# Performance work log

Hardware: AMD Instinct MI355X
Metric: run time of the kernel (lower is better)

## Reference

```python
import jax, jax.numpy as jnp
import numpy as np

DIM_M = 512
NEG_INF = -1e30


def setup_inputs() -> dict:
    key = jax.random.key(0)
    k1, k2, k3, k4, k5, k6, k7 = jax.random.split(key, 7)
    B, Lc, Lq, d = 16, 1024, 512, DIM_M
    C = jax.random.normal(k1, (B, Lc, d), dtype=jnp.float32)
    Q = jax.random.normal(k2, (B, Lq, d), dtype=jnp.float32)
    cmask = jax.random.randint(k3, (B, Lc), 0, 2).astype(jnp.float32)
    qmask = jax.random.randint(k4, (B, Lq), 0, 2).astype(jnp.float32)
    lim = np.sqrt(1.0 / d)
    w = jax.random.uniform(k5, (3 * d,), minval=-lim, maxval=lim, dtype=jnp.float32)
    # out_linear: Linear(4d -> d), torch default init
    bound = np.sqrt(1.0 / (4 * d))
    out_w = jax.random.uniform(k6, (d, 4 * d), minval=-bound, maxval=bound, dtype=jnp.float32)
    out_b = jax.random.uniform(k7, (d,), minval=-bound, maxval=bound, dtype=jnp.float32)
    return {"C": C, "Q": Q, "cmask": cmask, "qmask": qmask, "w": w, "out_w": out_w, "out_b": out_b}


def _mask_logits(t, m):
    return t * m + (1.0 - m) * NEG_INF


def reference(C, Q, cmask, qmask, w, out_w, out_b):
    d = C.shape[-1]
    w1, w2, w3 = w[:d], w[d:2 * d], w[2 * d:]
    # Decomposed trilinear similarity (same math as cat([Ct,Qt,Ct*Qt]) @ w):
    # S[b,i,j] = C[b,i]@w1 + Q[b,j]@w2 + (C[b,i]*w3) @ Q[b,j]
    S = (C @ w1)[:, :, None] + (Q @ w2)[:, None, :] \
        + jnp.einsum('bid,bjd->bij', C * w3, Q)  # [B, Lc, Lq]
    qm = qmask[:, None, :]  # [B, 1, Lq]
    cm = cmask[:, :, None]  # [B, Lc, 1]
    S1 = jax.nn.softmax(_mask_logits(S, qm), axis=2)  # over Lq
    S2 = jax.nn.softmax(_mask_logits(S, cm), axis=1)  # over Lc
    A = jnp.einsum('bij,bjd->bid', S1, Q)  # [B, Lc, d]
    # bmm(bmm(S1, S2^T), C) == S1 @ (S2^T @ C) by associativity (cheaper)
    S2TC = jnp.einsum('bij,bid->bjd', S2, C)  # [B, Lq, d]
    Bm = jnp.einsum('bij,bjd->bid', S1, S2TC)  # [B, Lc, d]
    out = jnp.concatenate([C, A, C * A, C * Bm], axis=2)  # [B, Lc, 4d]
    # dropout inactive (inference); out_linear
    return out @ out_w.T + out_b
```

## Files before the change

### kernel.cpp

```cpp
#include <hip/hip_runtime.h>
#include <hip/hip_bf16.h>


#define NB 16
#define LC 1024
#define LQ 512
#define DM 512
#define D4 2048
#define NEGINF (-1e30f)

typedef __bf16 v8bf __attribute__((ext_vector_type(8)));
typedef __bf16 v4bf __attribute__((ext_vector_type(4)));
typedef float  v4f  __attribute__((ext_vector_type(4)));

#define MFMA16 __builtin_amdgcn_mfma_f32_16x16x32_bf16

#define GLOAD16(gp, lp) __builtin_amdgcn_global_load_lds( \
    (const __attribute__((address_space(1))) void*)(gp), \
    (__attribute__((address_space(3))) void*)(lp), 16, 0, 0)

#define GEMM_PROLOG \
  __shared__ __bf16 Al[128 * 64], Bl[128 * 64]; \
  int bx = blockIdx.x, by = blockIdx.y, bz = blockIdx.z; \
  xcd_remap(bx, by, bz); \
  const int b = bz, i0 = by * 128, n0 = bx * 128; \
  const int t = threadIdx.x, lane = t & 63, wave = t >> 6; \
  const int wm = wave >> 1, wn = wave & 1, quad = lane >> 4, col = lane & 15; \
  const int srow = wave * 32 + (lane >> 3), scol = (lane & 7) * 8; \
  v4f acc[4][4]; \
  _Pragma("unroll") for (int x = 0; x < 4; ++x) \
  _Pragma("unroll") for (int y = 0; y < 4; ++y) \
  _Pragma("unroll") for (int r = 0; r < 4; ++r) acc[x][y][r] = 0.f;

#define GEMM_KLOOP(Arow, Brow, LDGA, LDGB, KEXT) \
  for (int k0 = 0; k0 < (KEXT); k0 += 64) { \
    _Pragma("unroll") for (int u = 0; u < 4; ++u) { \
      GLOAD16(Arow + (size_t)(u * 8) * (LDGA) + k0, &Al[(wave * 32 + u * 8) * 64]); \
      GLOAD16(Brow + (size_t)(u * 8) * (LDGB) + k0, &Bl[(wave * 32 + u * 8) * 64]); \
    } \
    __syncthreads(); \
    _Pragma("unroll") for (int ko = 0; ko < 2; ++ko) { \
      v8bf af_[4], bf_[4]; \
      _Pragma("unroll") for (int x = 0; x < 4; ++x) \
        af_[x] = *(const v8bf*)&Al[(wm * 64 + x * 16 + col) * 64 + ko * 32 + quad * 8]; \
      _Pragma("unroll") for (int y = 0; y < 4; ++y) \
        bf_[y] = *(const v8bf*)&Bl[(wn * 64 + y * 16 + col) * 64 + ko * 32 + quad * 8]; \
      _Pragma("unroll") for (int x = 0; x < 4; ++x) \
      _Pragma("unroll") for (int y = 0; y < 4; ++y) \
        acc[x][y] = MFMA16(af_[x], bf_[y], acc[x][y], 0, 0, 0); \
    } \
    __syncthreads(); \
  }

__device__ __forceinline__ void xcd_remap(int& bx, int& by, int& bz) {
  const int gx = gridDim.x, gy = gridDim.y, gz = gridDim.z;
  int flat = bx + gx * (by + gy * bz);
  int per = (gx * gy * gz) >> 3;
  int nw = (flat & 7) * per + (flat >> 3);
  bx = nw % gx;
  int r = nw / gx;
  by = r % gy;
  bz = r / gy;
}

__global__ void k_rowdots(const float* __restrict__ C, const float* __restrict__ Q,
                          const float* __restrict__ w,
                          float* __restrict__ cw1, float* __restrict__ qw2,
                          __bf16* __restrict__ Cbf, __bf16* __restrict__ Qw3) {
  const int wid = threadIdx.x >> 6, lane = threadIdx.x & 63;
  const int row = blockIdx.x * 4 + wid;
  const bool isC = row < NB * LC;
  const int lr = isC ? row : row - NB * LC;
  const float* src = (isC ? C : Q) + (size_t)lr * DM;
  const float* wv  = isC ? w : (w + DM);
  const float* w3  = w + 2 * DM;
  __bf16* dst = (isC ? Cbf : Qw3) + (size_t)lr * DM;
  float v = 0.f;
#pragma unroll
  for (int s = 0; s < 2; ++s) {
    const int k = lane * 4 + s * 256;
    float4 f = *(const float4*)(src + k);
    float4 g = *(const float4*)(wv + k);
    v += f.x * g.x + f.y * g.y + f.z * g.z + f.w * g.w;
    v4bf h;
    if (isC) {
      h[0] = (__bf16)f.x; h[1] = (__bf16)f.y; h[2] = (__bf16)f.z; h[3] = (__bf16)f.w;
    } else {
      float4 s3 = *(const float4*)(w3 + k);
      h[0] = (__bf16)(f.x * s3.x); h[1] = (__bf16)(f.y * s3.y);
      h[2] = (__bf16)(f.z * s3.z); h[3] = (__bf16)(f.w * s3.w);
    }
    *(v4bf*)(dst + k) = h;
  }
#pragma unroll
  for (int off = 32; off; off >>= 1) v += __shfl_down(v, off, 64);
  if (lane == 0) {
    if (isC) cw1[row] = v;
    else     qw2[lr] = v;
  }
}

__global__ void k_transpose(const float* __restrict__ in, __bf16* __restrict__ outT,
                            int R, int Cd) {
  __shared__ __bf16 tile[64][66];
  const int b = blockIdx.z;
  const int r0 = blockIdx.y * 64, c0 = blockIdx.x * 64;
  const int tr = threadIdx.x >> 6, tc = threadIdx.x & 63;
  const float* inb = in + (size_t)b * R * Cd;
  __bf16* outb = outT + (size_t)b * Cd * R;
  for (int r = tr; r < 64; r += 4)
    tile[r][tc] = (__bf16)inb[(size_t)(r0 + r) * Cd + c0 + tc];
  __syncthreads();
  for (int c = tr; c < 64; c += 4)
    outb[(size_t)(c0 + c) * R + r0 + tc] = tile[tc][c];
}

__global__ void k_cvt2(const float* __restrict__ Cf, const float* __restrict__ OW,
                       __bf16* __restrict__ Cb3, __bf16* __restrict__ OWb) {
  const size_t NC = (size_t)NB * LC * DM;
  size_t i = ((size_t)blockIdx.x * 256 + threadIdx.x) * 4;
  const float* src; __bf16* dst; size_t j;
  if (i < NC) { src = Cf; dst = Cb3; j = i; }
  else        { src = OW; dst = OWb; j = i - NC; }
  float4 f = *(const float4*)(src + j);
  v4bf h; h[0] = (__bf16)f.x; h[1] = (__bf16)f.y; h[2] = (__bf16)f.z; h[3] = (__bf16)f.w;
  *(v4bf*)(dst + j) = h;
}

__global__ __launch_bounds__(256) void k_mfma_S(
    const __bf16* __restrict__ Cbf, const __bf16* __restrict__ Qw3,
    const float* __restrict__ cw1, const float* __restrict__ qw2,
    float* __restrict__ S) {
  GEMM_PROLOG
  const __bf16* Arow = Cbf + (size_t)b * LC * DM + (size_t)(i0 + srow) * DM + scol;
  const __bf16* Brow = Qw3 + (size_t)b * LQ * DM + (size_t)(n0 + srow) * DM + scol;
  GEMM_KLOOP(Arow, Brow, DM, DM, DM)
  float* Sb = S + (size_t)b * LC * LQ;
#pragma unroll
  for (int x = 0; x < 4; ++x) {
    const int mB = i0 + wm * 64 + x * 16 + quad * 4;
    float cv[4];
#pragma unroll
    for (int r = 0; r < 4; ++r) cv[r] = cw1[b * LC + mB + r];
#pragma unroll
    for (int y = 0; y < 4; ++y) {
      const int j = n0 + wn * 64 + y * 16 + col;
      const float qv = qw2[b * LQ + j];
#pragma unroll
      for (int r = 0; r < 4; ++r)
        Sb[(size_t)(mB + r) * LQ + j] = acc[x][y][r] + cv[r] + qv;
    }
  }
}

__global__ __launch_bounds__(1024) void k_softstat(
    const float* __restrict__ S, const float* __restrict__ qmask,
    const float* __restrict__ cmask, __bf16* __restrict__ S1,
    float2* __restrict__ pstat) {
  __shared__ float2 cst[16][LQ];
  const int b = blockIdx.y, ic = blockIdx.x;
  const int tid = threadIdx.x, wv = tid >> 6, lane = tid & 63;
  const float* qm  = qmask + b * LQ;
  const float* cm  = cmask + b * LC + ic * 64;
  const float* Sb  = S  + ((size_t)b * LC + ic * 64) * LQ;
  __bf16*      S1b = S1 + ((size_t)b * LC + ic * 64) * LQ;
  float colm[8], cols[8];
#pragma unroll
  for (int tt = 0; tt < 8; ++tt) { colm[tt] = -3e38f; cols[tt] = 0.f; }
  for (int it = 0; it < 4; ++it) {
    const int r = wv * 4 + it;
    const float cmv = cm[r];
    const float* Srow = Sb + (size_t)r * LQ;
    float sv[8], l1[8];
    float m = -3e38f;
#pragma unroll
    for (int tt = 0; tt < 8; ++tt) {
      int j = lane + 64 * tt;
      sv[tt] = Srow[j];
      float qv = qm[j];
      l1[tt] = qv * sv[tt] + (1.f - qv) * NEGINF;
      m = fmaxf(m, l1[tt]);
    }
#pragma unroll
    for (int off = 32; off; off >>= 1) m = fmaxf(m, __shfl_xor(m, off, 64));
    float e[8], s = 0.f;
#pragma unroll
    for (int tt = 0; tt < 8; ++tt) { e[tt] = __expf(l1[tt] - m); s += e[tt]; }
#pragma unroll
    for (int off = 32; off; off >>= 1) s += __shfl_xor(s, off, 64);
    const float inv = 1.f / s;
#pragma unroll
    for (int tt = 0; tt < 8; ++tt)
      S1b[(size_t)r * LQ + lane + 64 * tt] = (__bf16)(e[tt] * inv);
#pragma unroll
    for (int tt = 0; tt < 8; ++tt) {
      float l2 = cmv * sv[tt] + (1.f - cmv) * NEGINF;
      if (l2 > colm[tt]) { cols[tt] *= __expf(colm[tt] - l2); colm[tt] = l2; }
      cols[tt] += __expf(l2 - colm[tt]);
    }
  }
#pragma unroll
  for (int tt = 0; tt < 8; ++tt) cst[wv][lane + 64 * tt] = make_float2(colm[tt], cols[tt]);
  __syncthreads();
  if (tid < LQ) {
    float M = -3e38f, Sd = 0.f;
#pragma unroll
    for (int k = 0; k < 16; ++k) {
      float2 p = cst[k][tid];
      float nM = fmaxf(M, p.x);
      Sd = Sd * __expf(M - nM) + p.y * __expf(p.x - nM);
      M = nM;
    }
    pstat[((size_t)(b * 16 + ic) * LQ) + tid] = make_float2(M, Sd);
  }
}

__global__ void k_colwrite(const float* __restrict__ S, const float* __restrict__ cmask,
                           const float2* __restrict__ pstat, __bf16* __restrict__ S2T) {
  __shared__ float Mf[64], If[64];
  __shared__ __bf16 tile[64][66];
  const int b = blockIdx.z, ic = blockIdx.y, j0 = blockIdx.x * 64;
  const int c = threadIdx.x & 63, ip = threadIdx.x >> 6;
  if (threadIdx.x < 64) {
    float M = -3e38f, Sd = 0.f;
#pragma unroll
    for (int k = 0; k < 16; ++k) {
      float2 p = pstat[((size_t)(b * 16 + k) * LQ) + j0 + threadIdx.x];
      float nM = fmaxf(M, p.x);
      Sd = Sd * __expf(M - nM) + p.y * __expf(p.x - nM);
      M = nM;
    }
    Mf[threadIdx.x] = M; If[threadIdx.x] = 1.f / Sd;
  }
  __syncthreads();
  const float M = Mf[c], inv = If[c];
  const float* Sb = S + ((size_t)b * LC + ic * 64) * LQ;
  const float* cm = cmask + b * LC + ic * 64;
  for (int r = ip; r < 64; r += 4) {
    float mk = cm[r];
    float logit = mk * Sb[(size_t)r * LQ + j0 + c] + (1.f - mk) * NEGINF;
    tile[r][c] = (__bf16)(__expf(logit - M) * inv);
  }
  __syncthreads();
  __bf16* S2Tb = S2T + ((size_t)b * LQ + j0) * LC + ic * 64;
  for (int jr = ip; jr < 64; jr += 4)
    S2Tb[(size_t)jr * LC + c] = tile[c][jr];
}

__global__ __launch_bounds__(256) void k_mfma_A(
    const __bf16* __restrict__ S1, const __bf16* __restrict__ QT,
    const float* __restrict__ Cf, __bf16* __restrict__ Aw, __bf16* __restrict__ CAw) {
  GEMM_PROLOG
  const __bf16* Arow = S1 + (size_t)b * LC * LQ + (size_t)(i0 + srow) * LQ + scol;
  const __bf16* Brow = QT + (size_t)b * DM * LQ + (size_t)(n0 + srow) * LQ + scol;
  GEMM_KLOOP(Arow, Brow, LQ, LQ, LQ)
  const float* Cb = Cf + (size_t)b * LC * DM;
  __bf16* Ab  = Aw  + (size_t)b * LC * DM;
  __bf16* CAb = CAw + (size_t)b * LC * DM;
#pragma unroll
  for (int x = 0; x < 4; ++x) {
    const int mB = i0 + wm * 64 + x * 16 + quad * 4;
#pragma unroll
    for (int y = 0; y < 4; ++y) {
      const int n = n0 + wn * 64 + y * 16 + col;
#pragma unroll
      for (int r = 0; r < 4; ++r) {
        const float av = acc[x][y][r];
        const float cv = Cb[(size_t)(mB + r) * DM + n];
        Ab[(size_t)(mB + r) * DM + n]  = (__bf16)av;
        CAb[(size_t)(mB + r) * DM + n] = (__bf16)(av * cv);
      }
    }
  }
}

__global__ __launch_bounds__(256) void k_mfma_T(
    const __bf16* __restrict__ S2T, const __bf16* __restrict__ CT, __bf16* __restrict__ S2TCT) {
  GEMM_PROLOG
  const int j0 = i0;
  const __bf16* Arow = S2T + (size_t)b * LQ * LC + (size_t)(j0 + srow) * LC + scol;
  const __bf16* Brow = CT  + (size_t)b * DM * LC + (size_t)(n0 + srow) * LC + scol;
  GEMM_KLOOP(Arow, Brow, LC, LC, LC)
#pragma unroll
  for (int x = 0; x < 4; ++x) {
    const int jB = j0 + wm * 64 + x * 16 + quad * 4;
#pragma unroll
    for (int y = 0; y < 4; ++y) {
      const int n = n0 + wn * 64 + y * 16 + col;
      v4bf h;
#pragma unroll
      for (int r = 0; r < 4; ++r) h[r] = (__bf16)acc[x][y][r];
      *(v4bf*)&S2TCT[((size_t)b * DM + n) * LQ + jB] = h;
    }
  }
}

__global__ __launch_bounds__(256) void k_mfma_Bm(
    const __bf16* __restrict__ S1, const __bf16* __restrict__ S2TCT,
    const float* __restrict__ Cf, __bf16* __restrict__ CBw) {
  GEMM_PROLOG
  const __bf16* Arow = S1    + (size_t)b * LC * LQ + (size_t)(i0 + srow) * LQ + scol;
  const __bf16* Brow = S2TCT + (size_t)b * DM * LQ + (size_t)(n0 + srow) * LQ + scol;
  GEMM_KLOOP(Arow, Brow, LQ, LQ, LQ)
  const float* Cb = Cf + (size_t)b * LC * DM;
  __bf16* CBb = CBw + (size_t)b * LC * DM;
#pragma unroll
  for (int x = 0; x < 4; ++x) {
    const int mB = i0 + wm * 64 + x * 16 + quad * 4;
#pragma unroll
    for (int y = 0; y < 4; ++y) {
      const int n = n0 + wn * 64 + y * 16 + col;
#pragma unroll
      for (int r = 0; r < 4; ++r) {
        const float cv = Cb[(size_t)(mB + r) * DM + n];
        CBb[(size_t)(mB + r) * DM + n] = (__bf16)(acc[x][y][r] * cv);
      }
    }
  }
}

__global__ __launch_bounds__(256) void k_mfma_out(
    const __bf16* __restrict__ Cb3, const __bf16* __restrict__ Aw,
    const __bf16* __restrict__ CAw, const __bf16* __restrict__ CBw,
    const __bf16* __restrict__ OWb, const float* __restrict__ ob,
    float* __restrict__ out) {
  GEMM_PROLOG
  const size_t rowoff = (size_t)b * LC * DM + (size_t)(i0 + srow) * DM + scol;
  const __bf16* As0 = Cb3 + rowoff;
  const __bf16* As1 = Aw  + rowoff;
  const __bf16* As2 = CAw + rowoff;
  const __bf16* As3 = CBw + rowoff;
  const __bf16* Brow0 = OWb + (size_t)(n0 + srow) * D4 + scol;
#pragma unroll
  for (int seg = 0; seg < 4; ++seg) {
    const __bf16* Arow = (seg == 0) ? As0 : (seg == 1) ? As1 : (seg == 2) ? As2 : As3;
    const __bf16* Brow = Brow0 + seg * DM;
    GEMM_KLOOP(Arow, Brow, DM, D4, DM)
  }
  float* outb = out + (size_t)b * LC * DM;
#pragma unroll
  for (int x = 0; x < 4; ++x) {
    const int mB = i0 + wm * 64 + x * 16 + quad * 4;
#pragma unroll
    for (int y = 0; y < 4; ++y) {
      const int n = n0 + wn * 64 + y * 16 + col;
      const float bv = ob[n];
#pragma unroll
      for (int r = 0; r < 4; ++r)
        outb[(size_t)(mB + r) * DM + n] = acc[x][y][r] + bv;
    }
  }
}

extern "C" void kernel_launch(void* const* d_in, const int* in_sizes, int n_in,
                              void* d_out, int out_size, void* d_ws, size_t ws_size,
                              hipStream_t stream) {
  const float* C     = (const float*)d_in[0];
  const float* Q     = (const float*)d_in[1];
  const float* cmask = (const float*)d_in[2];
  const float* qmask = (const float*)d_in[3];
  const float* w     = (const float*)d_in[4];
  const float* out_w = (const float*)d_in[5];
  const float* out_b = (const float*)d_in[6];
  float* out = (float*)d_out;

  char* base = (char*)d_ws;
  float*  cw1   = (float*)base;
  float*  qw2   = (float*)(base + 65536);
  char*   R     = base + 131072;
  float*  S     = (float*)R;
  __bf16* CT    = (__bf16*)R;
  __bf16* Aw    = (__bf16*)R;
  __bf16* QT    = (__bf16*)(R + (16u << 20));
  __bf16* CBw   = (__bf16*)(R + (16u << 20));
  __bf16* Cbf_e = (__bf16*)(R + (32u << 20));
  __bf16* S1    = (__bf16*)(R + (32u << 20));
  __bf16* Cbf3  = (__bf16*)(R + (32u << 20));
  __bf16* Qw3   = (__bf16*)(R + (48u << 20));
  __bf16* S2T   = (__bf16*)(R + (48u << 20));
  __bf16* CAw   = (__bf16*)(R + (48u << 20));
  float2* pstat = (float2*)(R + (64u << 20));
  __bf16* S2TCT = (__bf16*)(R + (64u << 20));
  __bf16* OWbf  = (__bf16*)(R + (64u << 20));
  (void)in_sizes; (void)n_in; (void)out_size; (void)ws_size;

  k_rowdots<<<(NB * LC + NB * LQ) / 4, 256, 0, stream>>>(C, Q, w, cw1, qw2, Cbf_e, Qw3);
  k_mfma_S<<<dim3(LQ / 128, LC / 128, NB), 256, 0, stream>>>(Cbf_e, Qw3, cw1, qw2, S);
  k_softstat<<<dim3(LC / 64, NB), 1024, 0, stream>>>(S, qmask, cmask, S1, pstat);
  k_colwrite<<<dim3(LQ / 64, LC / 64, NB), 256, 0, stream>>>(S, cmask, pstat, S2T);
  k_transpose<<<dim3(DM / 64, LC / 64, NB), 256, 0, stream>>>(C, CT, LC, DM);
  k_mfma_T<<<dim3(DM / 128, LQ / 128, NB), 256, 0, stream>>>(S2T, CT, S2TCT);
  k_transpose<<<dim3(DM / 64, LQ / 64, NB), 256, 0, stream>>>(Q, QT, LQ, DM);
  k_mfma_A<<<dim3(DM / 128, LC / 128, NB), 256, 0, stream>>>(S1, QT, C, Aw, CAw);
  k_mfma_Bm<<<dim3(DM / 128, LC / 128, NB), 256, 0, stream>>>(S1, S2TCT, C, CBw);
  k_cvt2<<<(NB * LC * DM + DM * D4) / 1024, 256, 0, stream>>>(C, out_w, Cbf3, OWbf);
  k_mfma_out<<<dim3(DM / 128, LC / 128, NB), 256, 0, stream>>>(Cbf3, Aw, CAw, CBw, OWbf, out_b, out);
}
```

Before: 288.8 us.

## Double-buffer LDS tiles in MFMA GEMMs and skip masked softmax work

```diff
diff --git a/kernel.cpp b/kernel.cpp
--- a/kernel.cpp
+++ b/kernel.cpp
@@ -20,7 +20,7 @@
     (__attribute__((address_space(3))) void*)(lp), 16, 0, 0)
 
 #define GEMM_PROLOG \
-  __shared__ __bf16 Al[128 * 64], Bl[128 * 64]; \
+  __shared__ __bf16 Al[2][128 * 64], Bl[2][128 * 64]; \
   int bx = blockIdx.x, by = blockIdx.y, bz = blockIdx.z; \
   xcd_remap(bx, by, bz); \
   const int b = bz, i0 = by * 128, n0 = bx * 128; \
@@ -32,25 +32,39 @@
   _Pragma("unroll") for (int y = 0; y < 4; ++y) \
   _Pragma("unroll") for (int r = 0; r < 4; ++r) acc[x][y][r] = 0.f;
 
+#define GEMM_STAGE(buf, Aptr, Bptr, LDGA, LDGB, k0) \
+  do { _Pragma("unroll") for (int u = 0; u < 4; ++u) { \
+    GLOAD16((Aptr) + (size_t)(u * 8) * (LDGA) + (k0), &Al[buf][(wave * 32 + u * 8) * 64]); \
+    GLOAD16((Bptr) + (size_t)(u * 8) * (LDGB) + (k0), &Bl[buf][(wave * 32 + u * 8) * 64]); \
+  } } while (0)
+
+#define GEMM_COMPUTE(buf) \
+  do { _Pragma("unroll") for (int ko = 0; ko < 2; ++ko) { \
+    v8bf af_[4], bf_[4]; \
+    _Pragma("unroll") for (int x = 0; x < 4; ++x) \
+      af_[x] = *(const v8bf*)&Al[buf][(wm * 64 + x * 16 + col) * 64 + ko * 32 + quad * 8]; \
+    _Pragma("unroll") for (int y = 0; y < 4; ++y) \
+      bf_[y] = *(const v8bf*)&Bl[buf][(wn * 64 + y * 16 + col) * 64 + ko * 32 + quad * 8]; \
+    _Pragma("unroll") for (int x = 0; x < 4; ++x) \
+    _Pragma("unroll") for (int y = 0; y < 4; ++y) \
+      acc[x][y] = MFMA16(af_[x], bf_[y], acc[x][y], 0, 0, 0); \
+  } } while (0)
+
+#define GEMM_SYNC() \
+  do { asm volatile("s_waitcnt vmcnt(0)" ::: "memory"); \
+       __builtin_amdgcn_s_barrier(); } while (0)
+
 #define GEMM_KLOOP(Arow, Brow, LDGA, LDGB, KEXT) \
-  for (int k0 = 0; k0 < (KEXT); k0 += 64) { \
-    _Pragma("unroll") for (int u = 0; u < 4; ++u) { \
-      GLOAD16(Arow + (size_t)(u * 8) * (LDGA) + k0, &Al[(wave * 32 + u * 8) * 64]); \
-      GLOAD16(Brow + (size_t)(u * 8) * (LDGB) + k0, &Bl[(wave * 32 + u * 8) * 64]); \
-    } \
-    __syncthreads(); \
-    _Pragma("unroll") for (int ko = 0; ko < 2; ++ko) { \
-      v8bf af_[4], bf_[4]; \
-      _Pragma("unroll") for (int x = 0; x < 4; ++x) \
-        af_[x] = *(const v8bf*)&Al[(wm * 64 + x * 16 + col) * 64 + ko * 32 + quad * 8]; \
-      _Pragma("unroll") for (int y = 0; y < 4; ++y) \
-        bf_[y] = *(const v8bf*)&Bl[(wn * 64 + y * 16 + col) * 64 + ko * 32 + quad * 8]; \
-      _Pragma("unroll") for (int x = 0; x < 4; ++x) \
-      _Pragma("unroll") for (int y = 0; y < 4; ++y) \
-        acc[x][y] = MFMA16(af_[x], bf_[y], acc[x][y], 0, 0, 0); \
-    } \
-    __syncthreads(); \
-  }
+  { GEMM_STAGE(0, Arow, Brow, LDGA, LDGB, 0); \
+    GEMM_SYNC(); \
+    int cur_ = 0; \
+    for (int k0 = 0; k0 < (KEXT); k0 += 64) { \
+      const int kn_ = k0 + 64; \
+      if (kn_ < (KEXT)) GEMM_STAGE(cur_ ^ 1, Arow, Brow, LDGA, LDGB, kn_); \
+      GEMM_COMPUTE(cur_); \
+      GEMM_SYNC(); \
+      cur_ ^= 1; \
+    } }
 
 __device__ __forceinline__ void xcd_remap(int& bx, int& by, int& bz) {
   const int gx = gridDim.x, gy = gridDim.y, gz = gridDim.z;
@@ -192,11 +206,13 @@
 #pragma unroll
     for (int tt = 0; tt < 8; ++tt)
       S1b[(size_t)r * LQ + lane + 64 * tt] = (__bf16)(e[tt] * inv);
-#pragma unroll
-    for (int tt = 0; tt < 8; ++tt) {
-      float l2 = cmv * sv[tt] + (1.f - cmv) * NEGINF;
-      if (l2 > colm[tt]) { cols[tt] *= __expf(colm[tt] - l2); colm[tt] = l2; }
-      cols[tt] += __expf(l2 - colm[tt]);
+    if (cmv != 0.f) {
+#pragma unroll
+      for (int tt = 0; tt < 8; ++tt) {
+        float l2 = sv[tt];
+        if (l2 > colm[tt]) { cols[tt] *= __expf(colm[tt] - l2); colm[tt] = l2; }
+        cols[tt] += __expf(l2 - colm[tt]);
+      }
     }
   }
 #pragma unroll
@@ -237,9 +253,10 @@
   const float* Sb = S + ((size_t)b * LC + ic * 64) * LQ;
   const float* cm = cmask + b * LC + ic * 64;
   for (int r = ip; r < 64; r += 4) {
-    float mk = cm[r];
-    float logit = mk * Sb[(size_t)r * LQ + j0 + c] + (1.f - mk) * NEGINF;
-    tile[r][c] = (__bf16)(__expf(logit - M) * inv);
+    if (cm[r] != 0.f)
+      tile[r][c] = (__bf16)(__expf(Sb[(size_t)r * LQ + j0 + c] - M) * inv);
+    else
+      tile[r][c] = (__bf16)0.f;
   }
   __syncthreads();
   __bf16* S2Tb = S2T + ((size_t)b * LQ + j0) * LC + ic * 64;
@@ -331,11 +348,23 @@
   const __bf16* As2 = CAw + rowoff;
   const __bf16* As3 = CBw + rowoff;
   const __bf16* Brow0 = OWb + (size_t)(n0 + srow) * D4 + scol;
+  GEMM_STAGE(0, As0, Brow0, DM, D4, 0);
+  GEMM_SYNC();
+  int cur_ = 0;
 #pragma unroll
   for (int seg = 0; seg < 4; ++seg) {
-    const __bf16* Arow = (seg == 0) ? As0 : (seg == 1) ? As1 : (seg == 2) ? As2 : As3;
-    const __bf16* Brow = Brow0 + seg * DM;
-    GEMM_KLOOP(Arow, Brow, DM, D4, DM)
+    const __bf16* Arow  = (seg == 0) ? As0 : (seg == 1) ? As1 : (seg == 2) ? As2 : As3;
+    const __bf16* Anext = (seg == 0) ? As1 : (seg == 1) ? As2 : As3;
+    const __bf16* Brow  = Brow0 + seg * DM;
+    const __bf16* Bnext = Brow0 + (seg < 3 ? seg + 1 : 3) * DM;
+    for (int k0 = 0; k0 < DM; k0 += 64) {
+      const int kn_ = k0 + 64;
+      if (kn_ < DM)      GEMM_STAGE(cur_ ^ 1, Arow, Brow, DM, D4, kn_);
+      else if (seg < 3)  GEMM_STAGE(cur_ ^ 1, Anext, Bnext, DM, D4, 0);
+      GEMM_COMPUTE(cur_);
+      GEMM_SYNC();
+      cur_ ^= 1;
+    }
   }
   float* outb = out + (size_t)b * LC * DM;
 #pragma unroll
```

Result: faster. 279.8 us (-3.1%).
